# Kernel tuning notes

Hardware: AMD Instinct MI355X
Metric: run time of the kernel (lower is better)

## Reference

```python
import jax, jax.numpy as jnp
import numpy as np

B, T, F, D, H, HD = 1, 16, 256, 768, 12, 64
NUM_LOOKBACK = 6  # remaining H - NUM_LOOKBACK heads are lookahead


def setup_inputs() -> dict:
    key = jax.random.key(0)
    ks = jax.random.split(key, 9)
    s = 0.02
    return {
        "x": jax.random.normal(ks[0], (B, T, F, D), dtype=jnp.float32),
        "Wq": jax.random.normal(ks[1], (H, D, HD), dtype=jnp.float32) * s,
        "bq": jax.random.normal(ks[2], (H, HD), dtype=jnp.float32) * s,
        "Wk": jax.random.normal(ks[3], (H, D, HD), dtype=jnp.float32) * s,
        "bk": jax.random.normal(ks[4], (H, HD), dtype=jnp.float32) * s,
        "Wv": jax.random.normal(ks[5], (H, D, HD), dtype=jnp.float32) * s,
        "bv": jax.random.normal(ks[6], (H, HD), dtype=jnp.float32) * s,
        "Wo": jax.random.normal(ks[7], (D, D), dtype=jnp.float32) * s,
        "bo": jax.random.normal(ks[8], (D,), dtype=jnp.float32) * s,
    }


def reference(x, Wq, bq, Wk, bk, Wv, bv, Wo, bo):
    b, t, f, d = x.shape
    tf = t * f
    xf = x.reshape(b, tf, d)

    # batched per-head projections: [b, h, n, hd]
    q = jnp.einsum('bnd,hdk->bhnk', xf, Wq) + bq[None, :, None, :]
    k = jnp.einsum('bnd,hdk->bhnk', xf, Wk) + bk[None, :, None, :]
    v = jnp.einsum('bnd,hdk->bhnk', xf, Wv) + bv[None, :, None, :]

    scale = 1.0 / jnp.sqrt(jnp.asarray(q.shape[-1], dtype=q.dtype))
    scores = jnp.einsum('bhqd,bhkd->bhqk', q, k) * scale  # [b,h,tf,tf]

    # lookback mask == causal (q_idx >= kv_idx); lookahead == anti-causal
    idx = jnp.arange(tf)
    causal = idx[:, None] >= idx[None, :]
    neg = jnp.finfo(scores.dtype).min
    s_lb = jnp.where(causal[None, None], scores[:, :NUM_LOOKBACK], neg)
    s_la = jnp.where(causal.T[None, None], scores[:, NUM_LOOKBACK:], neg)
    scores = jnp.concatenate([s_lb, s_la], axis=1)

    p = jax.nn.softmax(scores, axis=-1)
    o = jnp.einsum('bhqk,bhkd->bhqd', p, v)  # [b,h,tf,hd]
    o = o.transpose(0, 2, 1, 3).reshape(b, tf, d)  # concat heads on feature dim

    out = o @ Wo + bo
    return out.reshape(b, t, f, d)
```

## Files before the change

kernel.cpp:

```cpp
#include <hip/hip_runtime.h>
#include <hip/hip_bf16.h>

typedef __attribute__((ext_vector_type(4))) float f32x4;
typedef __attribute__((ext_vector_type(8))) short s16x8;
typedef __attribute__((ext_vector_type(4))) int i32x4;
typedef __attribute__((address_space(3))) unsigned char lds_t;
typedef __attribute__((address_space(1))) const unsigned char glob_t;

#define TFDIM 4096
#define DMODEL 768
#define NHEAD 12
#define HDIM 64
#define NLB 6
#define SLOTSZ 3145728

static __device__ __forceinline__ unsigned short f2bf(float f) {
    union { float f; unsigned u; } x; x.f = f;
    unsigned r = x.u + 0x7fff + ((x.u >> 16) & 1);
    return (unsigned short)(r >> 16);
}

static __device__ __forceinline__ float bf2f(unsigned short u) {
    return __uint_as_float(((unsigned)u) << 16);
}

static __device__ __forceinline__ float exp2_hw(float x) {
    float r;
    asm("v_exp_f32 %0, %1\n\ts_nop 0" : "=v"(r) : "v"(x));
    return r;
}

static __device__ __forceinline__ unsigned cvtpk_bf16(float lo, float hi) {
    unsigned r;
    asm("v_cvt_pk_bf16_f32 %0, %1, %2" : "=v"(r) : "v"(lo), "v"(hi));
    return r;
}

static __device__ __forceinline__ void xpose_pair(unsigned& a, unsigned& b) {
    asm volatile("v_permlane32_swap_b32 %0, %1" : "+v"(a), "+v"(b));
    asm volatile("v_permlane16_swap_b32 %0, %1" : "+v"(a), "+v"(b));
}

__global__ __launch_bounds__(256) void prep_kernel(
    const float* __restrict__ x, unsigned short* __restrict__ xb,
    const float* __restrict__ Wq, const float* __restrict__ Wk, const float* __restrict__ Wv,
    const float* __restrict__ bq, const float* __restrict__ bk, const float* __restrict__ bv,
    unsigned short* __restrict__ Wt, float* __restrict__ bias,
    const float* __restrict__ Wo, unsigned short* __restrict__ Wot,
    float* __restrict__ Lacc, float* __restrict__ Oacc) {
    __shared__ unsigned short tile[64][65];
    int b = blockIdx.x;
    int t = threadIdx.x;
    if (b < 432) {
        int qkv = b / 144, rem = b - qkv * 144, h = rem / 12, kt = rem - h * 12;
        const float* W = (qkv == 0) ? Wq : ((qkv == 1) ? Wk : Wv);
        int trow = t >> 2, tco = (t & 3) << 4;
        const float* src = &W[((size_t)h * 768 + kt * 64 + trow) * 64 + tco];
#pragma unroll
        for (int j = 0; j < 4; j++) {
            float4 v = *(const float4*)&src[j * 4];
            tile[trow][tco + j * 4 + 0] = f2bf(v.x);
            tile[trow][tco + j * 4 + 1] = f2bf(v.y);
            tile[trow][tco + j * 4 + 2] = f2bf(v.z);
            tile[trow][tco + j * 4 + 3] = f2bf(v.w);
        }
        if (kt == 0 && t < 64) {
            const float* bb = (qkv == 0) ? bq : ((qkv == 1) ? bk : bv);
            bias[qkv * 768 + h * 64 + t] = bb[h * 64 + t];
        }
        __syncthreads();
        unsigned short vals[16];
#pragma unroll
        for (int j = 0; j < 16; j++) vals[j] = tile[tco + j][trow];
        unsigned short* dst = &Wt[(size_t)(qkv * 768 + h * 64 + trow) * 768 + kt * 64 + tco];
        *(s16x8*)&dst[0] = *(const s16x8*)&vals[0];
        *(s16x8*)&dst[8] = *(const s16x8*)&vals[8];
    } else if (b < 576) {
        int bb = b - 432;
        int nt = bb / 12, kt = bb - nt * 12;
        int trow = t >> 2, tco = (t & 3) << 4;
        const float* src = &Wo[(size_t)(kt * 64 + trow) * 768 + nt * 64 + tco];
#pragma unroll
        for (int j = 0; j < 4; j++) {
            float4 v = *(const float4*)&src[j * 4];
            tile[trow][tco + j * 4 + 0] = f2bf(v.x);
            tile[trow][tco + j * 4 + 1] = f2bf(v.y);
            tile[trow][tco + j * 4 + 2] = f2bf(v.z);
            tile[trow][tco + j * 4 + 3] = f2bf(v.w);
        }
        __syncthreads();
        unsigned short vals[16];
#pragma unroll
        for (int j = 0; j < 16; j++) vals[j] = tile[tco + j][trow];
        unsigned short* dst = &Wot[(size_t)(nt * 64 + trow) * 768 + kt * 64 + tco];
        *(s16x8*)&dst[0] = *(const s16x8*)&vals[0];
        *(s16x8*)&dst[8] = *(const s16x8*)&vals[8];
    } else if (b < 624) {
        int i = (b - 576) * 256 + t;
        if (i < NHEAD * TFDIM / 4) {
            float4 z = {0.f, 0.f, 0.f, 0.f};
            ((float4*)Lacc)[i] = z;
        }
    } else if (b < 3696) {
        int i = (b - 624) * 256 + t;
        if (i < TFDIM * DMODEL / 4) {
            float4 v = ((const float4*)x)[i];
            ushort4 o;
            o.x = f2bf(v.x); o.y = f2bf(v.y); o.z = f2bf(v.z); o.w = f2bf(v.w);
            ((ushort4*)xb)[i] = o;
        }
    } else {
        int i = (b - 3696) * 256 + t;
        if (i < TFDIM * DMODEL / 4) {
            float4 z = {0.f, 0.f, 0.f, 0.f};
            ((float4*)Oacc)[i] = z;
        }
    }
}

template <int EPI, int ANORM>
__global__ __launch_bounds__(256) void gemm_bt_kernel(
    const unsigned short* __restrict__ A,
    const float* __restrict__ Af32, const float* __restrict__ Lacc,
    const unsigned short* __restrict__ Bt,
    const float* __restrict__ bias,
    float* __restrict__ Cf, unsigned short* __restrict__ Cb,
    unsigned short* __restrict__ Vtg,
    int M, int N, int K) {
    __shared__ __align__(16) unsigned short As[128 * 64];
    __shared__ __align__(16) unsigned short Bs[128 * 64];
    int tid = threadIdx.x;
    int w = tid >> 6, l = tid & 63, lr = l & 15, lg = l >> 4;
    int wm = w >> 1, wn = w & 1;

    int nwg = gridDim.x * gridDim.y;
    int flat = blockIdx.y * gridDim.x + blockIdx.x;
    int cpx = nwg >> 3;
    int swz = (flat & 7) * cpx + (flat >> 3);
    int bx = swz % gridDim.x, by = swz / gridDim.x;
    size_t mbase = (size_t)by * 128, nbase = (size_t)bx * 128;

    int drw = l >> 3, dslot = l & 7;
    int dg = (dslot ^ drw) << 3;
    f32x4 acc[4][4] = {};
    for (int k0 = 0; k0 < K; k0 += 64) {
        __syncthreads();
        if (ANORM) {
#pragma unroll
            for (int i = 0; i < 4; i++) {
                int idx = tid + i * 256;
                int row = idx >> 3, g = idx & 7;
                const float* src = &Af32[(mbase + row) * K + k0 + g * 8];
                float4 a0 = *(const float4*)&src[0];
                float4 a1 = *(const float4*)&src[4];
                float rl = __builtin_amdgcn_rcpf(Lacc[(size_t)(k0 >> 6) * TFDIM + mbase + row]);
                unsigned short us[8];
                us[0] = f2bf(a0.x * rl); us[1] = f2bf(a0.y * rl);
                us[2] = f2bf(a0.z * rl); us[3] = f2bf(a0.w * rl);
                us[4] = f2bf(a1.x * rl); us[5] = f2bf(a1.y * rl);
                us[6] = f2bf(a1.z * rl); us[7] = f2bf(a1.w * rl);
                *(s16x8*)&As[row * 64 + ((g ^ (row & 7)) << 3)] = *(const s16x8*)us;
            }
        } else {
#pragma unroll
            for (int j = 0; j < 4; j++) {
                int row = j * 32 + w * 8 + drw;
                __builtin_amdgcn_global_load_lds((glob_t*)&A[(mbase + row) * K + k0 + dg],
                                                 (lds_t*)&As[(j * 32 + w * 8) * 64], 16, 0, 0);
            }
        }
#pragma unroll
        for (int j = 0; j < 4; j++) {
            int row = j * 32 + w * 8 + drw;
            __builtin_amdgcn_global_load_lds((glob_t*)&Bt[(nbase + row) * K + k0 + dg],
                                             (lds_t*)&Bs[(j * 32 + w * 8) * 64], 16, 0, 0);
        }
        __syncthreads();
#pragma unroll
        for (int ks = 0; ks < 2; ks++) {
            s16x8 af[4], bfr[4];
#pragma unroll
            for (int m = 0; m < 4; m++) {
                int row = wm * 64 + m * 16 + lr;
                af[m] = *(const s16x8*)&As[row * 64 + (((ks * 4 + lg) ^ (row & 7)) << 3)];
            }
#pragma unroll
            for (int n = 0; n < 4; n++) {
                int row = wn * 64 + n * 16 + lr;
                bfr[n] = *(const s16x8*)&Bs[row * 64 + (((ks * 4 + lg) ^ (row & 7)) << 3)];
            }
#pragma unroll
            for (int m = 0; m < 4; m++)
#pragma unroll
                for (int n = 0; n < 4; n++)
                    acc[m][n] = __builtin_amdgcn_mfma_f32_16x16x32_bf16(af[m], bfr[n], acc[m][n], 0, 0, 0);
        }
    }
    if (EPI == 1 && nbase >= 1536) {
        __syncthreads();
        unsigned short* L = (w < 2) ? &As[w * 4096] : &Bs[(w - 2) * 4096];
#pragma unroll
        for (int n = 0; n < 4; n++) {
            int dloc = n * 16 + lr;
            float bv = bias[nbase + wn * 64 + dloc];
            int sw = (dloc & 7) << 3;
#pragma unroll
            for (int m = 0; m < 4; m++) {
                int tokloc = m * 16 + lg * 4;
                uint2 pw;
                pw.x = cvtpk_bf16(acc[m][n][0] + bv, acc[m][n][1] + bv);
                pw.y = cvtpk_bf16(acc[m][n][2] + bv, acc[m][n][3] + bv);
                *(uint2*)&L[dloc * 64 + (tokloc ^ sw)] = pw;
            }
        }
        __asm__ volatile("" ::: "memory");
        int hq = ((int)(nbase - 1536) >> 6) + wn;
        size_t vbase = (size_t)hq * 262144 + mbase + wm * 64;
#pragma unroll
        for (int it = 0; it < 8; it++) {
            int dl = it * 8 + (l >> 3);
            int t0 = (l & 7) * 8;
            s16x8 vv = *(const s16x8*)&L[dl * 64 + (t0 ^ ((dl & 7) << 3))];
            *(s16x8*)&Vtg[vbase + (size_t)dl * 4096 + t0] = vv;
        }
    } else {
#pragma unroll
        for (int m = 0; m < 4; m++) {
            size_t row0 = mbase + wm * 64 + m * 16 + lg * 4;
#pragma unroll
            for (int n = 0; n < 4; n++) {
                size_t col = nbase + wn * 64 + n * 16 + lr;
                float bv = bias[col];
#pragma unroll
                for (int r = 0; r < 4; r++) {
                    float v = acc[m][n][r] + bv;
                    if (EPI == 0) {
                        Cf[(row0 + r) * N + col] = v;
                    } else {
                        if (col < 768) v *= 0.18033688f;
                        Cb[(((col >> 6) * 4096 + (row0 + r)) << 6) + (col & 63)] = f2bf(v);
                    }
                }
            }
        }
    }
}

template <int PART>
__global__ __launch_bounds__(512, 4) void attn_kernel(const unsigned short* __restrict__ qk,
                                                      const unsigned short* __restrict__ vtg,
                                                      float* __restrict__ Oacc,
                                                      float* __restrict__ Lacc,
                                                      unsigned short* __restrict__ PO01,
                                                      unsigned short* __restrict__ PO23) {
    __shared__ __align__(16) unsigned short Ks[3][64][64];
    __shared__ __align__(16) unsigned short Vs[3][64][64];

    int b = blockIdx.x;
    int xc = b & 7, j = b >> 3;
    int t3 = j / 3, rsel = j - t3 * 3;
    int h, r;
    if (xc & 1) {
        int ffull = (3 * xc + 1) >> 1;
        if (rsel == 0)      { h = ffull;     r = 2 * t3; }
        else if (rsel == 1) { h = ffull;     r = 2 * t3 + 1; }
        else                { h = ffull - 1; r = 2 * t3 + 1; }
    } else {
        int ffull = (3 * xc) >> 1;
        if (rsel == 0)      { h = ffull;     r = 2 * t3; }
        else if (rsel == 1) { h = ffull;     r = 2 * t3 + 1; }
        else                { h = ffull + 1; r = 2 * t3; }
    }
    int idx = 79 - r;
    int jqw, c, n;
    if (idx < 8)       { jqw = idx;               c = 0;              n = 1; }
    else if (idx < 24) { jqw = 8 + ((idx - 8) >> 1);  c = (idx - 8) & 1;  n = 2; }
    else if (idx < 48) { jqw = 16 + (idx - 24) / 3;   c = (idx - 24) % 3; n = 3; }
    else               { jqw = 24 + ((idx - 48) >> 2); c = (idx - 48) & 3; n = 4; }
    int W = 2 * jqw + 2;
    int base = W / n, rem = W % n;
    int len = base + (c < rem ? 1 : 0);
    int s0 = c * base + (c < rem ? c : rem);
    bool causal = (h < NLB);
    int jq = causal ? jqw : (31 - jqw);
    int qbase = jq * 128;
    int dkb = 2 * jq;
    int kb0 = (causal ? 0 : (62 - 2 * jqw)) + s0;
    int kb1 = kb0 + len - 1;

    const unsigned short* Q  = qk + (size_t)h * TFDIM * HDIM;
    const unsigned short* Kp = qk + (size_t)(NHEAD + h) * TFDIM * HDIM;
    const unsigned short* Vt = vtg + (size_t)h * HDIM * TFDIM;

    int tid = threadIdx.x, w = tid >> 6, l = tid & 63, lr = l & 15, lg = l >> 4;
    int qh = w >> 2, wq = w & 3;
    int dk = dkb + qh;

    s16x8 qf[2];
    {
        size_t qrow = (size_t)(qbase + qh * 64 + wq * 16 + lr);
        qf[0] = *(const s16x8*)&Q[qrow * HDIM + lg * 8];
        qf[1] = *(const s16x8*)&Q[qrow * HDIM + 32 + lg * 8];
    }
    f32x4 oacc[4] = {};
    float lsum = 0.f;

    int drow = tid >> 3, dseg = tid & 7;
    int sg0 = (dseg ^ (drow & 7)) << 3;
    auto stage = [&](int buf, int kv) {
        __builtin_amdgcn_global_load_lds((glob_t*)(Kp + (size_t)(kv * 64 + drow) * HDIM + sg0),
                                         (lds_t*)&Ks[buf][w * 8][0], 16, 0, 0);
        __builtin_amdgcn_global_load_lds((glob_t*)(Vt + (size_t)drow * TFDIM + kv * 64 + sg0),
                                         (lds_t*)&Vs[buf][w * 8][0], 16, 0, 0);
    };

    stage(0, kb0);

    int cur = 0;
    int qcol = wq * 16 + lr;
    for (int kb = kb0; kb <= kb1; kb++) {
        bool more = (kb < kb1);
        if (more) {
            int nxt = (cur == 2) ? 0 : cur + 1;
            stage(nxt, kb + 1);
            asm volatile("s_waitcnt vmcnt(2)" ::: "memory");
        } else {
            asm volatile("s_waitcnt vmcnt(0)" ::: "memory");
        }
        __builtin_amdgcn_s_barrier();
        __builtin_amdgcn_sched_barrier(0);

        int kvbase = kb * 64;
        s16x8 vf[2][4];
#pragma unroll
        for (int ks = 0; ks < 2; ks++)
#pragma unroll
            for (int df = 0; df < 4; df++)
                vf[ks][df] = *(const s16x8*)&Vs[cur][df * 16 + lr][(ks * 32 + lg * 8) ^ ((lr & 7) << 3)];
        f32x4 s[4];
        __builtin_amdgcn_s_setprio(1);
#pragma unroll
        for (int f = 0; f < 4; f++) {
            s16x8 kf0 = *(const s16x8*)&Ks[cur][f * 16 + lr][(lg * 8) ^ ((lr & 7) << 3)];
            s16x8 kf1 = *(const s16x8*)&Ks[cur][f * 16 + lr][(32 + lg * 8) ^ ((lr & 7) << 3)];
            f32x4 z = {0.f, 0.f, 0.f, 0.f};
            z = __builtin_amdgcn_mfma_f32_16x16x32_bf16(kf0, qf[0], z, 0, 0, 0);
            z = __builtin_amdgcn_mfma_f32_16x16x32_bf16(kf1, qf[1], z, 0, 0, 0);
            s[f] = z;
        }
        __builtin_amdgcn_s_setprio(0);

        bool skip = causal ? (kb > dk) : (kb < dk);
        if (!skip) {
            if (kb == dk) {
                int qi = qbase + qh * 64 + qcol;
#pragma unroll
                for (int f = 0; f < 4; f++)
#pragma unroll
                    for (int r2 = 0; r2 < 4; r2++) {
                        int ki = kvbase + f * 16 + lg * 4 + r2;
                        bool keep = causal ? (qi >= ki) : (qi <= ki);
                        if (!keep) s[f][r2] = -1e30f;
                    }
            }
            float ls = 0.f;
            unsigned w0[4], w1[4];
#pragma unroll
            for (int f = 0; f < 4; f++) {
                float p0 = exp2_hw(s[f][0]);
                float p1 = exp2_hw(s[f][1]);
                float p2 = exp2_hw(s[f][2]);
                float p3 = exp2_hw(s[f][3]);
                ls += (p0 + p1) + (p2 + p3);
                w0[f] = cvtpk_bf16(p0, p1);
                w1[f] = cvtpk_bf16(p2, p3);
            }
            lsum += ls;
            xpose_pair(w0[0], w0[1]);
            xpose_pair(w1[0], w1[1]);
            xpose_pair(w0[2], w0[3]);
            xpose_pair(w1[2], w1[3]);
            union { unsigned u[4]; s16x8 v8; } pk0, pk1;
            pk0.u[0] = w0[0]; pk0.u[1] = w1[0]; pk0.u[2] = w0[1]; pk0.u[3] = w1[1];
            pk1.u[0] = w0[2]; pk1.u[1] = w1[2]; pk1.u[2] = w0[3]; pk1.u[3] = w1[3];
            __builtin_amdgcn_s_setprio(1);
#pragma unroll
            for (int df = 0; df < 4; df++) {
                oacc[df] = __builtin_amdgcn_mfma_f32_16x16x32_bf16(pk0.v8, vf[0][df], oacc[df], 0, 0, 0);
                oacc[df] = __builtin_amdgcn_mfma_f32_16x16x32_bf16(pk1.v8, vf[1][df], oacc[df], 0, 0, 0);
            }
            __builtin_amdgcn_s_setprio(0);
        }

        cur = (cur == 2) ? 0 : cur + 1;
    }
    lsum += __shfl_xor(lsum, 16);
    lsum += __shfl_xor(lsum, 32);
    if (lg == 0)
        atomicAdd(&Lacc[h * TFDIM + qbase + qh * 64 + wq * 16 + lr], lsum);
    if (PART) {
        unsigned short* PO = (c < 2) ? (PO01 + (size_t)c * SLOTSZ)
                                     : (PO23 + (size_t)(c - 2) * SLOTSZ);
#pragma unroll
        for (int df = 0; df < 4; df++)
#pragma unroll
            for (int r2 = 0; r2 < 4; r2++) {
                int row = qbase + qh * 64 + wq * 16 + lg * 4 + r2;
                PO[((size_t)h * TFDIM + row) * 64 + df * 16 + lr] = f2bf(oacc[df][r2]);
            }
    } else {
#pragma unroll
        for (int df = 0; df < 4; df++)
#pragma unroll
            for (int r2 = 0; r2 < 4; r2++) {
                int row = qbase + qh * 64 + wq * 16 + lg * 4 + r2;
                atomicAdd(&Oacc[(size_t)row * DMODEL + h * HDIM + df * 16 + lr], oacc[df][r2]);
            }
    }
}

__global__ void merge_kernel(const float* __restrict__ Oacc, const float* __restrict__ Lacc,
                             unsigned short* __restrict__ ob) {
    int i = blockIdx.x * 256 + threadIdx.x;
    if (i >= TFDIM * DMODEL / 4) return;
    int col4 = i % (DMODEL / 4), row = i / (DMODEL / 4);
    float4 v = ((const float4*)Oacc)[i];
    int h = col4 >> 4;
    float rl = 1.0f / Lacc[h * TFDIM + row];
    ushort4 u;
    u.x = f2bf(v.x * rl); u.y = f2bf(v.y * rl); u.z = f2bf(v.z * rl); u.w = f2bf(v.w * rl);
    ((ushort4*)ob)[i] = u;
}

__global__ void merge_part_kernel(const unsigned short* __restrict__ PO01,
                                  const unsigned short* __restrict__ PO23,
                                  const float* __restrict__ Lacc,
                                  unsigned short* __restrict__ ob) {
    int i = blockIdx.x * 256 + threadIdx.x;
    if (i >= TFDIM * 96) return;
    int row = i / 96, g = i - row * 96;
    int h = g >> 3, c0 = (g & 7) << 3;
    int jq = row >> 7;
    int jqw = (h < NLB) ? jq : (31 - jq);
    int n = 1 + (jqw >> 3);
    size_t off = ((size_t)h * TFDIM + row) * 64 + c0;
    float acc[8] = {};
    for (int s = 0; s < n; s++) {
        const unsigned short* PO = (s < 2) ? (PO01 + (size_t)s * SLOTSZ)
                                           : (PO23 + (size_t)(s - 2) * SLOTSZ);
        s16x8 v = *(const s16x8*)&PO[off];
#pragma unroll
        for (int j = 0; j < 8; j++) acc[j] += bf2f((unsigned short)v[j]);
    }
    float rl = 1.0f / Lacc[h * TFDIM + row];
    unsigned short o8[8];
#pragma unroll
    for (int j = 0; j < 8; j++) o8[j] = f2bf(acc[j] * rl);
    *(s16x8*)&ob[(size_t)row * DMODEL + h * HDIM + c0] = *(const s16x8*)o8;
}


extern "C" void kernel_launch(void* const* d_in, const int* in_sizes, int n_in,
                              void* d_out, int out_size, void* d_ws, size_t ws_size,
                              hipStream_t stream) {
    const float* x  = (const float*)d_in[0];
    const float* Wq = (const float*)d_in[1];
    const float* bq = (const float*)d_in[2];
    const float* Wk = (const float*)d_in[3];
    const float* bk = (const float*)d_in[4];
    const float* Wv = (const float*)d_in[5];
    const float* bv = (const float*)d_in[6];
    const float* Wo = (const float*)d_in[7];
    const float* bo = (const float*)d_in[8];
    float* out = (float*)d_out;
    char* ws = (char*)d_ws;
    const unsigned short* dummyA = (const unsigned short*)d_ws;

    if (ws_size >= 45416448) {
        unsigned short* xb     = (unsigned short*)(ws + 0);
        unsigned short* PO01   = (unsigned short*)(ws + 0);
        unsigned short* WtQ    = (unsigned short*)(ws + 6291456);
        float*          bqkv   = (float*)(ws + 9830400);
        unsigned short* qkb    = (unsigned short*)(ws + 12582912);
        unsigned short* ob2    = (unsigned short*)(ws + 12582912);
        unsigned short* vtg    = (unsigned short*)(ws + 25165824);
        unsigned short* Wot    = (unsigned short*)(ws + 31457280);
        float*          Lacc   = (float*)(ws + 32636928);
        unsigned short* PO23   = (unsigned short*)(ws + 32833536);

        prep_kernel<<<3696, 256, 0, stream>>>(x, xb, Wq, Wk, Wv, bq, bk, bv, WtQ, bqkv, Wo, Wot, Lacc, nullptr);

        dim3 g1(2304 / 128, 4096 / 128);
        gemm_bt_kernel<1, 0><<<g1, 256, 0, stream>>>(xb, nullptr, nullptr, WtQ, bqkv, nullptr, qkb, vtg, 4096, 2304, 768);

        attn_kernel<1><<<960, 512, 0, stream>>>(qkb, vtg, nullptr, Lacc, PO01, PO23);

        merge_part_kernel<<<(TFDIM * 96 + 255) / 256, 256, 0, stream>>>(PO01, PO23, Lacc, ob2);

        dim3 g3(768 / 128, 4096 / 128);
        gemm_bt_kernel<0, 0><<<g3, 256, 0, stream>>>(ob2, nullptr, nullptr, Wot, bo, out, nullptr, nullptr, 4096, 768, 768);
    } else if (ws_size >= 32833536) {
        float*          Oacc = (float*)(ws + 0);
        unsigned short* xb   = (unsigned short*)(ws + 0);
        unsigned short* WtQ  = (unsigned short*)(ws + 6291456);
        float*          bqkv = (float*)(ws + 9830400);
        unsigned short* qkb  = (unsigned short*)(ws + 12582912);
        unsigned short* ob2  = (unsigned short*)(ws + 12582912);
        unsigned short* vtg  = (unsigned short*)(ws + 25165824);
        unsigned short* Wot  = (unsigned short*)(ws + 31457280);
        float*          Lacc = (float*)(ws + 32636928);

        prep_kernel<<<3696, 256, 0, stream>>>(x, xb, Wq, Wk, Wv, bq, bk, bv, WtQ, bqkv, Wo, Wot, Lacc, nullptr);

        dim3 g1(2304 / 128, 4096 / 128);
        gemm_bt_kernel<1, 0><<<g1, 256, 0, stream>>>(xb, nullptr, nullptr, WtQ, bqkv, nullptr, qkb, vtg, 4096, 2304, 768);

        hipMemsetAsync(Oacc, 0, (size_t)TFDIM * DMODEL * 4, stream);

        attn_kernel<0><<<960, 512, 0, stream>>>(qkb, vtg, Oacc, Lacc, nullptr, nullptr);

        merge_kernel<<<(TFDIM * DMODEL / 4 + 255) / 256, 256, 0, stream>>>(Oacc, Lacc, ob2);

        dim3 g3(768 / 128, 4096 / 128);
        gemm_bt_kernel<0, 0><<<g3, 256, 0, stream>>>(ob2, nullptr, nullptr, Wot, bo, out, nullptr, nullptr, 4096, 768, 768);
    } else {
        unsigned short* xb   = (unsigned short*)(ws + 0);
        unsigned short* ob   = (unsigned short*)(ws + 0);
        unsigned short* WtQ  = (unsigned short*)(ws + 6291456);
        unsigned short* Wot  = (unsigned short*)(ws + 9830400);
        float*          bqkv = (float*)(ws + 11010048);
        unsigned short* qkb  = (unsigned short*)(ws + 11019264);
        unsigned short* vtg  = (unsigned short*)(ws + 23602176);
        float*          Lacc = (float*)(ws + 29893632);
        float*          Oacc = out;

        hipMemsetAsync(Oacc, 0, (size_t)TFDIM * DMODEL * 4, stream);
        prep_kernel<<<3696, 256, 0, stream>>>(x, xb, Wq, Wk, Wv, bq, bk, bv, WtQ, bqkv, Wo, Wot, Lacc, nullptr);

        dim3 g1(2304 / 128, 4096 / 128);
        gemm_bt_kernel<1, 0><<<g1, 256, 0, stream>>>(xb, nullptr, nullptr, WtQ, bqkv, nullptr, qkb, vtg, 4096, 2304, 768);

        attn_kernel<0><<<960, 512, 0, stream>>>(qkb, vtg, Oacc, Lacc, nullptr, nullptr);
        merge_kernel<<<(TFDIM * DMODEL / 4 + 255) / 256, 256, 0, stream>>>(Oacc, Lacc, ob);

        dim3 g3(768 / 128, 4096 / 128);
        gemm_bt_kernel<0, 0><<<g3, 256, 0, stream>>>(ob, nullptr, nullptr, Wot, bo, out, nullptr, nullptr, 4096, 768, 768);
    }
}
```

Measured before the change: 107.7 us.

## Fuse partial-output merge into output-projection GEMM A-tile load

```diff
diff --git a/kernel.cpp b/kernel.cpp
--- a/kernel.cpp
+++ b/kernel.cpp
@@ -118,10 +118,11 @@
     }
 }
 
-template <int EPI, int ANORM>
+template <int EPI, int AX>
 __global__ __launch_bounds__(256) void gemm_bt_kernel(
     const unsigned short* __restrict__ A,
-    const float* __restrict__ Af32, const float* __restrict__ Lacc,
+    const unsigned short* __restrict__ PO01, const unsigned short* __restrict__ PO23,
+    const float* __restrict__ LaccM,
     const unsigned short* __restrict__ Bt,
     const float* __restrict__ bias,
     float* __restrict__ Cf, unsigned short* __restrict__ Cb,
@@ -145,20 +146,28 @@
     f32x4 acc[4][4] = {};
     for (int k0 = 0; k0 < K; k0 += 64) {
         __syncthreads();
-        if (ANORM) {
+        if (AX == 2) {
+            int h = k0 >> 6;
+            int jq = (int)(mbase >> 7);
+            int jqw = (h < NLB) ? jq : 31 - jq;
+            int n = 1 + (jqw >> 3);
 #pragma unroll
             for (int i = 0; i < 4; i++) {
                 int idx = tid + i * 256;
                 int row = idx >> 3, g = idx & 7;
-                const float* src = &Af32[(mbase + row) * K + k0 + g * 8];
-                float4 a0 = *(const float4*)&src[0];
-                float4 a1 = *(const float4*)&src[4];
-                float rl = __builtin_amdgcn_rcpf(Lacc[(size_t)(k0 >> 6) * TFDIM + mbase + row]);
+                size_t off = ((size_t)(h * TFDIM) + mbase + row) * 64 + g * 8;
+                float accv[8] = {};
+                for (int s = 0; s < n; s++) {
+                    const unsigned short* PO = (s < 2) ? (PO01 + (size_t)s * SLOTSZ)
+                                                       : (PO23 + (size_t)(s - 2) * SLOTSZ);
+                    s16x8 v = *(const s16x8*)&PO[off];
+#pragma unroll
+                    for (int j2 = 0; j2 < 8; j2++) accv[j2] += bf2f((unsigned short)v[j2]);
+                }
+                float rl = __builtin_amdgcn_rcpf(LaccM[h * TFDIM + mbase + row]);
                 unsigned short us[8];
-                us[0] = f2bf(a0.x * rl); us[1] = f2bf(a0.y * rl);
-                us[2] = f2bf(a0.z * rl); us[3] = f2bf(a0.w * rl);
-                us[4] = f2bf(a1.x * rl); us[5] = f2bf(a1.y * rl);
-                us[6] = f2bf(a1.z * rl); us[7] = f2bf(a1.w * rl);
+#pragma unroll
+                for (int j2 = 0; j2 < 8; j2++) us[j2] = f2bf(accv[j2] * rl);
                 *(s16x8*)&As[row * 64 + ((g ^ (row & 7)) << 3)] = *(const s16x8*)us;
             }
         } else {
@@ -185,31 +194,31 @@
                 af[m] = *(const s16x8*)&As[row * 64 + (((ks * 4 + lg) ^ (row & 7)) << 3)];
             }
 #pragma unroll
-            for (int n = 0; n < 4; n++) {
-                int row = wn * 64 + n * 16 + lr;
-                bfr[n] = *(const s16x8*)&Bs[row * 64 + (((ks * 4 + lg) ^ (row & 7)) << 3)];
+            for (int n2 = 0; n2 < 4; n2++) {
+                int row = wn * 64 + n2 * 16 + lr;
+                bfr[n2] = *(const s16x8*)&Bs[row * 64 + (((ks * 4 + lg) ^ (row & 7)) << 3)];
             }
 #pragma unroll
             for (int m = 0; m < 4; m++)
 #pragma unroll
-                for (int n = 0; n < 4; n++)
-                    acc[m][n] = __builtin_amdgcn_mfma_f32_16x16x32_bf16(af[m], bfr[n], acc[m][n], 0, 0, 0);
+                for (int n2 = 0; n2 < 4; n2++)
+                    acc[m][n2] = __builtin_amdgcn_mfma_f32_16x16x32_bf16(af[m], bfr[n2], acc[m][n2], 0, 0, 0);
         }
     }
     if (EPI == 1 && nbase >= 1536) {
         __syncthreads();
         unsigned short* L = (w < 2) ? &As[w * 4096] : &Bs[(w - 2) * 4096];
 #pragma unroll
-        for (int n = 0; n < 4; n++) {
-            int dloc = n * 16 + lr;
+        for (int n2 = 0; n2 < 4; n2++) {
+            int dloc = n2 * 16 + lr;
             float bv = bias[nbase + wn * 64 + dloc];
             int sw = (dloc & 7) << 3;
 #pragma unroll
             for (int m = 0; m < 4; m++) {
                 int tokloc = m * 16 + lg * 4;
                 uint2 pw;
-                pw.x = cvtpk_bf16(acc[m][n][0] + bv, acc[m][n][1] + bv);
-                pw.y = cvtpk_bf16(acc[m][n][2] + bv, acc[m][n][3] + bv);
+                pw.x = cvtpk_bf16(acc[m][n2][0] + bv, acc[m][n2][1] + bv);
+                pw.y = cvtpk_bf16(acc[m][n2][2] + bv, acc[m][n2][3] + bv);
                 *(uint2*)&L[dloc * 64 + (tokloc ^ sw)] = pw;
             }
         }
@@ -228,12 +237,12 @@
         for (int m = 0; m < 4; m++) {
             size_t row0 = mbase + wm * 64 + m * 16 + lg * 4;
 #pragma unroll
-            for (int n = 0; n < 4; n++) {
-                size_t col = nbase + wn * 64 + n * 16 + lr;
+            for (int n2 = 0; n2 < 4; n2++) {
+                size_t col = nbase + wn * 64 + n2 * 16 + lr;
                 float bv = bias[col];
 #pragma unroll
                 for (int r = 0; r < 4; r++) {
-                    float v = acc[m][n][r] + bv;
+                    float v = acc[m][n2][r] + bv;
                     if (EPI == 0) {
                         Cf[(row0 + r) * N + col] = v;
                     } else {
@@ -432,33 +441,6 @@
     ((ushort4*)ob)[i] = u;
 }
 
-__global__ void merge_part_kernel(const unsigned short* __restrict__ PO01,
-                                  const unsigned short* __restrict__ PO23,
-                                  const float* __restrict__ Lacc,
-                                  unsigned short* __restrict__ ob) {
-    int i = blockIdx.x * 256 + threadIdx.x;
-    if (i >= TFDIM * 96) return;
-    int row = i / 96, g = i - row * 96;
-    int h = g >> 3, c0 = (g & 7) << 3;
-    int jq = row >> 7;
-    int jqw = (h < NLB) ? jq : (31 - jq);
-    int n = 1 + (jqw >> 3);
-    size_t off = ((size_t)h * TFDIM + row) * 64 + c0;
-    float acc[8] = {};
-    for (int s = 0; s < n; s++) {
-        const unsigned short* PO = (s < 2) ? (PO01 + (size_t)s * SLOTSZ)
-                                           : (PO23 + (size_t)(s - 2) * SLOTSZ);
-        s16x8 v = *(const s16x8*)&PO[off];
-#pragma unroll
-        for (int j = 0; j < 8; j++) acc[j] += bf2f((unsigned short)v[j]);
-    }
-    float rl = 1.0f / Lacc[h * TFDIM + row];
-    unsigned short o8[8];
-#pragma unroll
-    for (int j = 0; j < 8; j++) o8[j] = f2bf(acc[j] * rl);
-    *(s16x8*)&ob[(size_t)row * DMODEL + h * HDIM + c0] = *(const s16x8*)o8;
-}
-
 
 extern "C" void kernel_launch(void* const* d_in, const int* in_sizes, int n_in,
                               void* d_out, int out_size, void* d_ws, size_t ws_size,
@@ -482,7 +464,6 @@
         unsigned short* WtQ    = (unsigned short*)(ws + 6291456);
         float*          bqkv   = (float*)(ws + 9830400);
         unsigned short* qkb    = (unsigned short*)(ws + 12582912);
-        unsigned short* ob2    = (unsigned short*)(ws + 12582912);
         unsigned short* vtg    = (unsigned short*)(ws + 25165824);
         unsigned short* Wot    = (unsigned short*)(ws + 31457280);
         float*          Lacc   = (float*)(ws + 32636928);
@@ -491,14 +472,12 @@
         prep_kernel<<<3696, 256, 0, stream>>>(x, xb, Wq, Wk, Wv, bq, bk, bv, WtQ, bqkv, Wo, Wot, Lacc, nullptr);
 
         dim3 g1(2304 / 128, 4096 / 128);
-        gemm_bt_kernel<1, 0><<<g1, 256, 0, stream>>>(xb, nullptr, nullptr, WtQ, bqkv, nullptr, qkb, vtg, 4096, 2304, 768);
+        gemm_bt_kernel<1, 0><<<g1, 256, 0, stream>>>(xb, nullptr, nullptr, nullptr, WtQ, bqkv, nullptr, qkb, vtg, 4096, 2304, 768);
 
         attn_kernel<1><<<960, 512, 0, stream>>>(qkb, vtg, nullptr, Lacc, PO01, PO23);
 
-        merge_part_kernel<<<(TFDIM * 96 + 255) / 256, 256, 0, stream>>>(PO01, PO23, Lacc, ob2);
-
         dim3 g3(768 / 128, 4096 / 128);
-        gemm_bt_kernel<0, 0><<<g3, 256, 0, stream>>>(ob2, nullptr, nullptr, Wot, bo, out, nullptr, nullptr, 4096, 768, 768);
+        gemm_bt_kernel<0, 2><<<g3, 256, 0, stream>>>(dummyA, PO01, PO23, Lacc, Wot, bo, out, nullptr, nullptr, 4096, 768, 768);
     } else if (ws_size >= 32833536) {
         float*          Oacc = (float*)(ws + 0);
         unsigned short* xb   = (unsigned short*)(ws + 0);
@@ -513,7 +492,7 @@
         prep_kernel<<<3696, 256, 0, stream>>>(x, xb, Wq, Wk, Wv, bq, bk, bv, WtQ, bqkv, Wo, Wot, Lacc, nullptr);
 
         dim3 g1(2304 / 128, 4096 / 128);
-        gemm_bt_kernel<1, 0><<<g1, 256, 0, stream>>>(xb, nullptr, nullptr, WtQ, bqkv, nullptr, qkb, vtg, 4096, 2304, 768);
+        gemm_bt_kernel<1, 0><<<g1, 256, 0, stream>>>(xb, nullptr, nullptr, nullptr, WtQ, bqkv, nullptr, qkb, vtg, 4096, 2304, 768);
 
         hipMemsetAsync(Oacc, 0, (size_t)TFDIM * DMODEL * 4, stream);
 
@@ -522,7 +501,7 @@
         merge_kernel<<<(TFDIM * DMODEL / 4 + 255) / 256, 256, 0, stream>>>(Oacc, Lacc, ob2);
 
         dim3 g3(768 / 128, 4096 / 128);
-        gemm_bt_kernel<0, 0><<<g3, 256, 0, stream>>>(ob2, nullptr, nullptr, Wot, bo, out, nullptr, nullptr, 4096, 768, 768);
+        gemm_bt_kernel<0, 0><<<g3, 256, 0, stream>>>(ob2, nullptr, nullptr, nullptr, Wot, bo, out, nullptr, nullptr, 4096, 768, 768);
     } else {
         unsigned short* xb   = (unsigned short*)(ws + 0);
         unsigned short* ob   = (unsigned short*)(ws + 0);
@@ -538,12 +517,12 @@
         prep_kernel<<<3696, 256, 0, stream>>>(x, xb, Wq, Wk, Wv, bq, bk, bv, WtQ, bqkv, Wo, Wot, Lacc, nullptr);
 
         dim3 g1(2304 / 128, 4096 / 128);
-        gemm_bt_kernel<1, 0><<<g1, 256, 0, stream>>>(xb, nullptr, nullptr, WtQ, bqkv, nullptr, qkb, vtg, 4096, 2304, 768);
+        gemm_bt_kernel<1, 0><<<g1, 256, 0, stream>>>(xb, nullptr, nullptr, nullptr, WtQ, bqkv, nullptr, qkb, vtg, 4096, 2304, 768);
 
         attn_kernel<0><<<960, 512, 0, stream>>>(qkb, vtg, Oacc, Lacc, nullptr, nullptr);
         merge_kernel<<<(TFDIM * DMODEL / 4 + 255) / 256, 256, 0, stream>>>(Oacc, Lacc, ob);
 
         dim3 g3(768 / 128, 4096 / 128);
-        gemm_bt_kernel<0, 0><<<g3, 256, 0, stream>>>(ob, nullptr, nullptr, Wot, bo, out, nullptr, nullptr, 4096, 768, 768);
-    }
-}
+        gemm_bt_kernel<0, 0><<<g3, 256, 0, stream>>>(ob, nullptr, nullptr, nullptr, Wot, bo, out, nullptr, nullptr, 4096, 768, 768);
+    }
+}
```

After: 140.6 us. 1.3x slower.
